# Kernel tuning notes

Measured on AMD Instinct MI355X. Metric: run time of the kernel, lower is better.

Reference implementation:

```python
import jax, jax.numpy as jnp
import numpy as np

# Single-rank simulation of all_to_all_vdev_2d_offset (MoE token combine).
NUM_RANKS = 1
NUM_LOCAL_EXPERTS = 8
NSPLITS = NUM_RANKS * NUM_LOCAL_EXPERTS
IN_LEN = 16384
OUT_LEN = 16384
HIDDEN = 4096
SPLIT = IN_LEN // NSPLITS  # 2048 tokens per (rank, expert) chunk


def setup_inputs() -> dict:
    key = jax.random.key(0)
    k1, _ = jax.random.split(key)
    inp = jax.random.normal(k1, (IN_LEN, HIDDEN), dtype=jnp.float32)
    out = jnp.zeros((OUT_LEN, HIDDEN), dtype=jnp.float32)
    splits = np.full(NSPLITS, SPLIT, dtype=np.int64)
    # Input chunks laid out in reversed expert order -> non-trivial shuffle.
    perm = np.arange(NSPLITS)[::-1]
    in_off = (perm * SPLIT).astype(np.int64)
    out_off = (np.arange(NSPLITS) * SPLIT).astype(np.int64)  # sorted (rank-major)
    in_splits_offsets = jnp.asarray(np.stack([splits, in_off]))
    out_splits_offsets = jnp.asarray(np.stack([splits, out_off]))
    return {
        "inp": inp,
        "out": out,
        "in_splits_offsets": in_splits_offsets,
        "out_splits_offsets": out_splits_offsets,
    }


def reference(inp, out, in_splits_offsets, out_splits_offsets):
    """Copy chunk j (in_splits[j] rows) from input offset in_off[j] to output
    offset out_off[j]; output rows outside any chunk keep the `out` buffer value."""
    in_off = in_splits_offsets[1]
    out_splits = out_splits_offsets[0]
    out_off = out_splits_offsets[1]  # assumed sorted (rank-major layout)
    out_len = out.shape[0]
    r = jnp.arange(out_len)
    # chunk id owning each output row
    j = jnp.clip(jnp.searchsorted(out_off, r, side="right") - 1, 0, out_off.shape[0] - 1)
    pos = r - out_off[j]                      # offset within chunk
    valid = pos < out_splits[j]               # rows beyond split are padding
    src = jnp.clip(in_off[j] + pos, 0, inp.shape[0] - 1)
    return jnp.where(valid[:, None], inp[src], out)
```

## Files before the change

### kernel.cpp

```cpp
#include <hip/hip_runtime.h>


__global__ __launch_bounds__(256) void TokenCombiner_70523363000736_kernel(
    const float4* __restrict__ inp,
    const float4* __restrict__ outbuf,
    const int*    __restrict__ in_so,
    const int*    __restrict__ out_so,
    float4*       __restrict__ out,
    int nsplits, int hidden4, int in_rows)
{
    const int row = blockIdx.x;

    const int* out_splits = out_so;
    const int* out_off    = out_so + nsplits;
    const int* in_off     = in_so  + nsplits;

    int j = 0;
    #pragma unroll 8
    for (int k = 1; k < nsplits; ++k)
        if (out_off[k] <= row) j = k;

    const int  pos   = row - out_off[j];
    const bool valid = pos < out_splits[j];

    long src = (long)in_off[j] + (long)pos;
    if (src < 0) src = 0;
    if (src > (long)(in_rows - 1)) src = (long)(in_rows - 1);

    const float4* src_row = valid ? (inp + src * (long)hidden4)
                                  : (outbuf + (long)row * (long)hidden4);
    float4* dst_row = out + (long)row * (long)hidden4;

    for (int c = threadIdx.x; c < hidden4; c += blockDim.x)
        dst_row[c] = src_row[c];
}

extern "C" void kernel_launch(void* const* d_in, const int* in_sizes, int n_in,
                              void* d_out, int out_size, void* d_ws, size_t ws_size,
                              hipStream_t stream) {
    const float4* inp    = (const float4*)d_in[0];
    const float4* outbuf = (const float4*)d_in[1];
    const int*    in_so  = (const int*)d_in[2];
    const int*    out_so = (const int*)d_in[3];
    float4*       out    = (float4*)d_out;

    const int hidden   = 4096;
    const int hidden4  = hidden / 4;
    const int nsplits  = in_sizes[2] / 2;
    const int in_rows  = in_sizes[0] / hidden;
    const int out_rows = out_size   / hidden;

    TokenCombiner_70523363000736_kernel<<<out_rows, 256, 0, stream>>>(
        inp, outbuf, in_so, out_so, out, nsplits, hidden4, in_rows);
}
```

Before: 533.2 us.

## Process eight rows per block with unrolled nontemporal vector loads and stores

Each block now copies eight output rows instead of one, and hidden is fixed at compile time so every thread issues four independent 16-byte loads before four stores per row. The loads and stores use nontemporal builtins so the streamed copy bypasses normal cache retention. The aim is more memory-level parallelism per thread and less per-block launch and index overhead on a purely bandwidth-bound copy. In exchange the grid is eight times smaller, and hidden=4096 is hardcoded.

```diff
diff --git a/kernel.cpp b/kernel.cpp
--- a/kernel.cpp
+++ b/kernel.cpp
@@ -1,55 +1,74 @@
 #include <hip/hip_runtime.h>
 
 
-__global__ __launch_bounds__(256) void TokenCombiner_70523363000736_kernel(
-    const float4* __restrict__ inp,
-    const float4* __restrict__ outbuf,
-    const int*    __restrict__ in_so,
-    const int*    __restrict__ out_so,
-    float4*       __restrict__ out,
-    int nsplits, int hidden4, int in_rows)
+typedef float f4 __attribute__((ext_vector_type(4)));
+
+constexpr int H4  = 1024;
+constexpr int RPB = 8;
+constexpr int TPB = 256;
+
+__global__ __launch_bounds__(TPB) void TokenCombiner_70523363000736_kernel(
+    const f4* __restrict__ inp,
+    const f4* __restrict__ outbuf,
+    const int* __restrict__ in_so,
+    const int* __restrict__ out_so,
+    f4*       __restrict__ out,
+    int nsplits, int in_rows, int out_rows)
 {
-    const int row = blockIdx.x;
+    const int r0 = blockIdx.x * RPB;
+    const int t  = threadIdx.x;
 
     const int* out_splits = out_so;
     const int* out_off    = out_so + nsplits;
     const int* in_off     = in_so  + nsplits;
 
-    int j = 0;
-    #pragma unroll 8
-    for (int k = 1; k < nsplits; ++k)
-        if (out_off[k] <= row) j = k;
+    #pragma unroll
+    for (int i = 0; i < RPB; ++i) {
+        const int row = r0 + i;
+        if (row < out_rows) {
+            int j = 0;
+            for (int k = 1; k < nsplits; ++k)
+                if (out_off[k] <= row) j = k;
 
-    const int  pos   = row - out_off[j];
-    const bool valid = pos < out_splits[j];
+            const int  pos   = row - out_off[j];
+            const bool valid = pos < out_splits[j];
 
-    long src = (long)in_off[j] + (long)pos;
-    if (src < 0) src = 0;
-    if (src > (long)(in_rows - 1)) src = (long)(in_rows - 1);
+            long src = (long)in_off[j] + (long)pos;
+            if (src < 0) src = 0;
+            if (src > (long)(in_rows - 1)) src = (long)(in_rows - 1);
 
-    const float4* src_row = valid ? (inp + src * (long)hidden4)
-                                  : (outbuf + (long)row * (long)hidden4);
-    float4* dst_row = out + (long)row * (long)hidden4;
+            const f4* __restrict__ s = valid ? (inp + src * (long)H4)
+                                             : (outbuf + (long)row * (long)H4);
+            f4* __restrict__ d = out + (long)row * (long)H4;
 
-    for (int c = threadIdx.x; c < hidden4; c += blockDim.x)
-        dst_row[c] = src_row[c];
+            f4 v0 = __builtin_nontemporal_load(&s[t + 0 * TPB]);
+            f4 v1 = __builtin_nontemporal_load(&s[t + 1 * TPB]);
+            f4 v2 = __builtin_nontemporal_load(&s[t + 2 * TPB]);
+            f4 v3 = __builtin_nontemporal_load(&s[t + 3 * TPB]);
+            __builtin_nontemporal_store(v0, &d[t + 0 * TPB]);
+            __builtin_nontemporal_store(v1, &d[t + 1 * TPB]);
+            __builtin_nontemporal_store(v2, &d[t + 2 * TPB]);
+            __builtin_nontemporal_store(v3, &d[t + 3 * TPB]);
+        }
+    }
 }
 
 extern "C" void kernel_launch(void* const* d_in, const int* in_sizes, int n_in,
                               void* d_out, int out_size, void* d_ws, size_t ws_size,
                               hipStream_t stream) {
-    const float4* inp    = (const float4*)d_in[0];
-    const float4* outbuf = (const float4*)d_in[1];
-    const int*    in_so  = (const int*)d_in[2];
-    const int*    out_so = (const int*)d_in[3];
-    float4*       out    = (float4*)d_out;
+    const f4*  inp    = (const f4*)d_in[0];
+    const f4*  outbuf = (const f4*)d_in[1];
+    const int* in_so  = (const int*)d_in[2];
+    const int* out_so = (const int*)d_in[3];
+    f4*        out    = (f4*)d_out;
 
     const int hidden   = 4096;
-    const int hidden4  = hidden / 4;
     const int nsplits  = in_sizes[2] / 2;
     const int in_rows  = in_sizes[0] / hidden;
     const int out_rows = out_size   / hidden;
 
-    TokenCombiner_70523363000736_kernel<<<out_rows, 256, 0, stream>>>(
-        inp, outbuf, in_so, out_so, out, nsplits, hidden4, in_rows);
+    const int grid = (out_rows + RPB - 1) / RPB;
+
+    TokenCombiner_70523363000736_kernel<<<grid, TPB, 0, stream>>>(
+        inp, outbuf, in_so, out_so, out, nsplits, in_rows, out_rows);
 }
```

New measurement: 532.3 us. About the same (-0.2%).
